# Performance work log

Measured on AMD Instinct MI355X. Metric: run time of the kernel, lower is better.

Reference implementation:

```python
import jax, jax.numpy as jnp
import numpy as np

N_EMB = 768
HEAD_SIZE = 64
B, T = 256, 256


def setup_inputs() -> dict:
    key = jax.random.key(0)
    kx, kq, kk, kv = jax.random.split(key, 4)
    x = jax.random.normal(kx, (B, T, N_EMB), dtype=jnp.float32)
    # nn.Linear(n_emb, head_size, bias=False): store as [in, out], apply x @ W
    s = 1.0 / np.sqrt(N_EMB)
    Wq = jax.random.uniform(kq, (N_EMB, HEAD_SIZE), jnp.float32, -s, s)
    Wk = jax.random.uniform(kk, (N_EMB, HEAD_SIZE), jnp.float32, -s, s)
    Wv = jax.random.uniform(kv, (N_EMB, HEAD_SIZE), jnp.float32, -s, s)
    return {"x": x, "Wq": Wq, "Wk": Wk, "Wv": Wv}


def reference(x, Wq, Wk, Wv):
    # x: [B, T, C]
    q = x @ Wq  # [B, T, H]
    k = x @ Wk  # [B, T, H]
    v = x @ Wv  # [B, T, H]
    scale = k.shape[-1] ** (-0.5)
    wei = jnp.einsum('bth,bsh->bts', q, k) * scale  # [B, T, T]
    t = x.shape[1]
    causal = jnp.tril(jnp.ones((t, t), dtype=bool))  # [T, T]
    wei = jnp.where(causal, wei, -jnp.inf)
    wei = jax.nn.softmax(wei, axis=-1)
    out = jnp.einsum('bts,bsh->bth', wei, v)  # [B, T, H]
    return out
```

## Files before the change

kernel.cpp:

```cpp
#include <hip/hip_runtime.h>
#include <hip/hip_bf16.h>
#include <stdint.h>


typedef __attribute__((ext_vector_type(8))) short short8;
typedef __attribute__((ext_vector_type(4))) short short4v;
typedef __attribute__((ext_vector_type(4))) float f32x4;

#define MFMA16(a, b, c) __builtin_amdgcn_mfma_f32_16x16x32_bf16(a, b, c, 0, 0, 0)

#define BAR() do { \
  asm volatile("s_waitcnt lgkmcnt(0)" ::: "memory"); \
  __builtin_amdgcn_s_barrier(); \
} while (0)

static __device__ __forceinline__ unsigned short f2bf(float f) {
  union { float f; uint32_t u; } v; v.f = f;
  return (unsigned short)((v.u + 0x7FFFu + ((v.u >> 16) & 1u)) >> 16);
}

__global__ void wt_prep(const float* __restrict__ Wq, const float* __restrict__ Wk,
                        const float* __restrict__ Wv, unsigned short* __restrict__ WtT) {
  int idx = blockIdx.x * 256 + threadIdx.x;
  if (idx >= 147456) return;
  int co = idx & 63;
  int c = (idx >> 6) & 31;
  int itm = idx >> 11;
  int it = itm / 3;
  int m = itm - it * 3;
  const float* W = (m == 0) ? Wq : (m == 1 ? Wk : Wv);
  float v = W[(it * 32 + c) * 64 + co];
  if (m == 0) v *= 0.125f;
  WtT[it * 7680 + (m * 64 + co) * 40 + c] = f2bf(v);
}

#define XS0 0
#define XS1 20480
#define WS0 40960
#define WS1 56320
#define KOFF 71680
#define VOFF 104448

__global__ __launch_bounds__(1024, 1) void fused_head(
    const float* __restrict__ x, const unsigned short* __restrict__ WtT,
    float* __restrict__ out) {
  __shared__ char smem[137216];
  const int tid = threadIdx.x;
  const int w = tid >> 6;
  const int lane = tid & 63;
  const int l15 = lane & 15, g = lane >> 4;
  const int b = blockIdx.x;
  const float* xB = x + (size_t)b * 256 * 768;

  char* xs0 = smem + XS0;
  char* xs1 = smem + XS1;
  char* ws0 = smem + WS0;
  char* ws1 = smem + WS1;

  f32x4 acc[12];
  #pragma unroll
  for (int ct = 0; ct < 12; ++ct) acc[ct] = f32x4{0.f, 0.f, 0.f, 0.f};

  const int sxr = tid >> 3;
  const int sxc = tid & 7;
  const bool stv = (tid < 480);

  float4 xA[2], xPB[2];
  short8 wA[2], wPB[2];

  auto loadX = [&](float4* xr, int kk) {
    #pragma unroll
    for (int p = 0; p < 2; ++p)
      xr[p] = *reinterpret_cast<const float4*>(
          xB + (size_t)(p * 128 + sxr) * 768 + kk + sxc * 4);
  };
  auto loadW = [&](short8* wr, int it) {
    if (stv) {
      const short8* s = reinterpret_cast<const short8*>(WtT + (size_t)it * 7680 + tid * 16);
      wr[0] = s[0]; wr[1] = s[1];
    }
  };
  auto storeX = [&](char* xsb, const float4* xr) {
    #pragma unroll
    for (int p = 0; p < 2; ++p) {
      short4v v;
      v[0] = (short)f2bf(xr[p].x); v[1] = (short)f2bf(xr[p].y);
      v[2] = (short)f2bf(xr[p].z); v[3] = (short)f2bf(xr[p].w);
      *reinterpret_cast<short4v*>(xsb + (p * 128 + sxr) * 80 + sxc * 8) = v;
    }
  };
  auto storeW = [&](char* wsb, const short8* wr) {
    if (stv) {
      *reinterpret_cast<short8*>(wsb + tid * 32) = wr[0];
      *reinterpret_cast<short8*>(wsb + tid * 32 + 16) = wr[1];
    }
  };
  auto compute = [&](const char* xsb, const char* wsb) {
    short8 a0 = *reinterpret_cast<const short8*>(xsb + (w * 16 + l15) * 80 + g * 16);
    #pragma unroll
    for (int ct = 0; ct < 12; ++ct) {
      short8 bb = *reinterpret_cast<const short8*>(wsb + (ct * 16 + l15) * 80 + g * 16);
      acc[ct] = MFMA16(a0, bb, acc[ct]);
    }
  };

  loadX(xA, 0); loadW(wA, 0);
  storeX(xs0, xA); storeW(ws0, wA);
  loadX(xPB, 32); loadW(wPB, 1);
  BAR();

  for (int j = 0; j < 12; ++j) {
    if (2 * j + 2 < 24) { loadX(xA, (2 * j + 2) * 32); loadW(wA, 2 * j + 2); }
    compute(xs0, ws0);
    storeX(xs1, xPB); storeW(ws1, wPB);
    BAR();
    if (2 * j + 3 < 24) { loadX(xPB, (2 * j + 3) * 32); loadW(wPB, 2 * j + 3); }
    compute(xs1, ws1);
    if (2 * j + 2 < 24) { storeX(xs0, xA); storeW(ws0, wA); }
    BAR();
  }

  char* Kl = smem + KOFF;
  char* Vl = smem + VOFF;
  char* Ql = smem;
  #pragma unroll
  for (int ct = 0; ct < 4; ++ct) {
    #pragma unroll
    for (int r = 0; r < 4; ++r) {
      int key = w * 16 + g * 4 + r;
      int h = ct * 16 + l15;
      *reinterpret_cast<unsigned short*>(
          Kl + key * 128 + ((h * 2) ^ ((key & 7) << 4))) = f2bf(acc[4 + ct][r]);
      *reinterpret_cast<unsigned short*>(
          Ql + key * 256 + ((h * 2) ^ ((key & 15) << 4))) = f2bf(acc[ct][r]);
    }
    int h = ct * 16 + l15;
    int t0 = w * 16 + g * 4;
    short4v pv;
    pv[0] = (short)f2bf(acc[8 + ct][0]); pv[1] = (short)f2bf(acc[8 + ct][1]);
    pv[2] = (short)f2bf(acc[8 + ct][2]); pv[3] = (short)f2bf(acc[8 + ct][3]);
    *reinterpret_cast<short4v*>(Vl + h * 512 + ((t0 * 2) ^ ((h & 7) << 4))) = pv;
  }
  BAR();

  short8 qf[2][2];
  if (w < 8) {
    #pragma unroll
    for (int rt = 0; rt < 2; ++rt) {
      const int qrow0 = (rt == 0) ? w * 16 : (15 - w) * 16;
      #pragma unroll
      for (int c = 0; c < 2; ++c) {
        int row = qrow0 + l15;
        qf[rt][c] = *reinterpret_cast<const short8*>(
            Ql + row * 256 + ((c * 64 + g * 16) ^ ((row & 15) << 4)));
      }
    }
  }
  BAR();

  if (w < 8) {
    char* Pw = smem + w * 8192;

    #pragma unroll
    for (int rt = 0; rt < 2; ++rt) {
      const int tile_idx = (rt == 0) ? w : 15 - w;
      const int trow0 = tile_idx * 16;
      const int ntile = tile_idx + 1;
      const int pswz = (l15 & 7) << 4;

      f32x4 s[16];
      #pragma unroll
      for (int t = 0; t < 16; ++t) {
        if (t < ntile) {
          int key = t * 16 + l15;
          int kswz = (key & 7) << 4;
          short8 k0 = *reinterpret_cast<const short8*>(Kl + key * 128 + ((g * 16) ^ kswz));
          short8 k1 = *reinterpret_cast<const short8*>(Kl + key * 128 + ((64 + g * 16) ^ kswz));
          f32x4 a = f32x4{0.f, 0.f, 0.f, 0.f};
          a = MFMA16(k0, qf[rt][0], a);
          a = MFMA16(k1, qf[rt][1], a);
          s[t] = a;
        }
      }

      float sum = 0.f;
      #pragma unroll
      for (int t = 0; t < 16; ++t) {
        if (t < ntile) {
          const bool diag = (t == ntile - 1);
          short4v pk;
          #pragma unroll
          for (int r = 0; r < 4; ++r) {
            float p = __expf(s[t][r]);
            if (diag && (g * 4 + r > l15)) p = 0.f;
            sum += p;
            pk[r] = (short)f2bf(p);
          }
          *reinterpret_cast<short4v*>(Pw + l15 * 512 + ((t * 32 + g * 8) ^ pswz)) = pk;
        }
      }
      if (ntile & 1) {
        *reinterpret_cast<short4v*>(Pw + l15 * 512 + ((ntile * 32 + g * 8) ^ pswz)) =
            short4v{0, 0, 0, 0};
      }
      sum += __shfl_xor(sum, 16);
      sum += __shfl_xor(sum, 32);
      const float inv = 1.0f / sum;

      const int nkc = (ntile + 1) >> 1;
      f32x4 o[4];
      #pragma unroll
      for (int i = 0; i < 4; ++i) o[i] = f32x4{0.f, 0.f, 0.f, 0.f};
      #pragma unroll
      for (int kc = 0; kc < 8; ++kc) {
        if (kc < nkc) {
          short8 pa = *reinterpret_cast<const short8*>(
              Pw + l15 * 512 + ((kc * 64 + g * 16) ^ pswz));
          #pragma unroll
          for (int ht = 0; ht < 4; ++ht) {
            int h = ht * 16 + l15;
            short8 bv = *reinterpret_cast<const short8*>(
                Vl + h * 512 + ((kc * 64 + g * 16) ^ ((h & 7) << 4)));
            o[ht] = MFMA16(bv, pa, o[ht]);
          }
        }
      }

      float* dst = out + ((size_t)b * 256 + trow0 + l15) * 64 + g * 4;
      #pragma unroll
      for (int ht = 0; ht < 4; ++ht) {
        float4 ov;
        ov.x = o[ht][0] * inv; ov.y = o[ht][1] * inv;
        ov.z = o[ht][2] * inv; ov.w = o[ht][3] * inv;
        *reinterpret_cast<float4*>(dst + ht * 16) = ov;
      }
    }
  }
}

extern "C" void kernel_launch(void* const* d_in, const int* in_sizes, int n_in,
                              void* d_out, int out_size, void* d_ws, size_t ws_size,
                              hipStream_t stream) {
  const float* x  = (const float*)d_in[0];
  const float* Wq = (const float*)d_in[1];
  const float* Wk = (const float*)d_in[2];
  const float* Wv = (const float*)d_in[3];
  unsigned short* WtT = (unsigned short*)d_ws;
  float* out = (float*)d_out;

  hipLaunchKernelGGL(wt_prep, dim3(576), dim3(256), 0, stream, Wq, Wk, Wv, WtT);
  hipLaunchKernelGGL(fused_head, dim3(256), dim3(1024), 0, stream, x, WtT, out);
}
```

Measured before the change: 51.14 us.

## Split fused head into separate projection and attention kernels via global bf16 buffers

Replaces the single fused 1024-thread-per-batch kernel with a projection kernel and an attention kernel. The projection kernel handles 128 rows per block across 512 blocks, writing Q, K and transposed V as bf16 to workspace. The attention kernel, with 512 threads per batch, reloads them into LDS. This is meant to raise occupancy and parallelism in the projection phase, where 256 single-occupancy blocks underfill the GPU and half the waves sat idle during attention. In exchange it adds a global round trip of Q/K/V and an extra kernel launch.

```diff
diff --git a/kernel.cpp b/kernel.cpp
--- a/kernel.cpp
+++ b/kernel.cpp
@@ -17,6 +17,15 @@
 static __device__ __forceinline__ unsigned short f2bf(float f) {
   union { float f; uint32_t u; } v; v.f = f;
   return (unsigned short)((v.u + 0x7FFFu + ((v.u >> 16) & 1u)) >> 16);
+}
+
+static __device__ __forceinline__ short8 conv8(float4 lo, float4 hi) {
+  short8 a;
+  a[0] = (short)f2bf(lo.x); a[1] = (short)f2bf(lo.y);
+  a[2] = (short)f2bf(lo.z); a[3] = (short)f2bf(lo.w);
+  a[4] = (short)f2bf(hi.x); a[5] = (short)f2bf(hi.y);
+  a[6] = (short)f2bf(hi.z); a[7] = (short)f2bf(hi.w);
+  return a;
 }
 
 __global__ void wt_prep(const float* __restrict__ Wq, const float* __restrict__ Wk,
@@ -34,45 +43,37 @@
   WtT[it * 7680 + (m * 64 + co) * 40 + c] = f2bf(v);
 }
 
-#define XS0 0
-#define XS1 20480
-#define WS0 40960
-#define WS1 56320
-#define KOFF 71680
-#define VOFF 104448
-
-__global__ __launch_bounds__(1024, 1) void fused_head(
+__global__ __launch_bounds__(512, 4) void proj_kernel(
     const float* __restrict__ x, const unsigned short* __restrict__ WtT,
-    float* __restrict__ out) {
-  __shared__ char smem[137216];
+    unsigned short* __restrict__ Q, unsigned short* __restrict__ Kb,
+    unsigned short* __restrict__ Vt) {
+  __shared__ char smem[51200];
+  char* xs_[2] = { smem, smem + 10240 };
+  char* ws_[2] = { smem + 20480, smem + 35840 };
+
   const int tid = threadIdx.x;
-  const int w = tid >> 6;
-  const int lane = tid & 63;
+  const int w = tid >> 6, lane = tid & 63;
   const int l15 = lane & 15, g = lane >> 4;
-  const int b = blockIdx.x;
-  const float* xB = x + (size_t)b * 256 * 768;
-
-  char* xs0 = smem + XS0;
-  char* xs1 = smem + XS1;
-  char* ws0 = smem + WS0;
-  char* ws1 = smem + WS1;
+  const int bid = blockIdx.x;
+  const int b = bid >> 1;
+  const int row0 = (bid & 1) * 128;
+  const float* xB = x + ((size_t)b * 256 + row0) * 768;
 
   f32x4 acc[12];
   #pragma unroll
   for (int ct = 0; ct < 12; ++ct) acc[ct] = f32x4{0.f, 0.f, 0.f, 0.f};
 
-  const int sxr = tid >> 3;
-  const int sxc = tid & 7;
+  const int sxr = tid >> 2;
+  const int sxc = tid & 3;
   const bool stv = (tid < 480);
 
   float4 xA[2], xPB[2];
   short8 wA[2], wPB[2];
 
   auto loadX = [&](float4* xr, int kk) {
-    #pragma unroll
-    for (int p = 0; p < 2; ++p)
-      xr[p] = *reinterpret_cast<const float4*>(
-          xB + (size_t)(p * 128 + sxr) * 768 + kk + sxc * 4);
+    const float* src = xB + (size_t)sxr * 768 + kk + sxc * 8;
+    xr[0] = *reinterpret_cast<const float4*>(src);
+    xr[1] = *reinterpret_cast<const float4*>(src + 4);
   };
   auto loadW = [&](short8* wr, int it) {
     if (stv) {
@@ -81,13 +82,7 @@
     }
   };
   auto storeX = [&](char* xsb, const float4* xr) {
-    #pragma unroll
-    for (int p = 0; p < 2; ++p) {
-      short4v v;
-      v[0] = (short)f2bf(xr[p].x); v[1] = (short)f2bf(xr[p].y);
-      v[2] = (short)f2bf(xr[p].z); v[3] = (short)f2bf(xr[p].w);
-      *reinterpret_cast<short4v*>(xsb + (p * 128 + sxr) * 80 + sxc * 8) = v;
-    }
+    *reinterpret_cast<short8*>(xsb + sxr * 80 + sxc * 16) = conv8(xr[0], xr[1]);
   };
   auto storeW = [&](char* wsb, const short8* wr) {
     if (stv) {
@@ -105,135 +100,157 @@
   };
 
   loadX(xA, 0); loadW(wA, 0);
-  storeX(xs0, xA); storeW(ws0, wA);
+  storeX(xs_[0], xA); storeW(ws_[0], wA);
   loadX(xPB, 32); loadW(wPB, 1);
   BAR();
 
   for (int j = 0; j < 12; ++j) {
     if (2 * j + 2 < 24) { loadX(xA, (2 * j + 2) * 32); loadW(wA, 2 * j + 2); }
-    compute(xs0, ws0);
-    storeX(xs1, xPB); storeW(ws1, wPB);
+    compute(xs_[0], ws_[0]);
+    storeX(xs_[1], xPB); storeW(ws_[1], wPB);
     BAR();
     if (2 * j + 3 < 24) { loadX(xPB, (2 * j + 3) * 32); loadW(wPB, 2 * j + 3); }
-    compute(xs1, ws1);
-    if (2 * j + 2 < 24) { storeX(xs0, xA); storeW(ws0, wA); }
+    compute(xs_[1], ws_[1]);
+    if (2 * j + 2 < 24) { storeX(xs_[0], xA); storeW(ws_[0], wA); }
     BAR();
   }
+
+  {
+    const int trow_l = row0 + w * 16 + g * 4;
+    #pragma unroll
+    for (int ct = 0; ct < 4; ++ct) {
+      #pragma unroll
+      for (int r = 0; r < 4; ++r) {
+        size_t base = ((size_t)b * 256 + trow_l + r) * 64 + l15;
+        Q[base + ct * 16] = f2bf(acc[ct][r]);
+        Kb[base + ct * 16] = f2bf(acc[4 + ct][r]);
+      }
+      int h = ct * 16 + l15;
+      short4v pv;
+      pv[0] = (short)f2bf(acc[8 + ct][0]); pv[1] = (short)f2bf(acc[8 + ct][1]);
+      pv[2] = (short)f2bf(acc[8 + ct][2]); pv[3] = (short)f2bf(acc[8 + ct][3]);
+      *reinterpret_cast<short4v*>(&Vt[((size_t)b * 64 + h) * 256 + trow_l]) = pv;
+    }
+  }
+}
+
+#define KOFF 65536
+#define VOFF 98304
+__global__ __launch_bounds__(512, 2) void attn_kernel(
+    const unsigned short* __restrict__ Q, const unsigned short* __restrict__ Kb,
+    const unsigned short* __restrict__ Vt, float* __restrict__ out) {
+  __shared__ char smem[131072];
+  const int tid = threadIdx.x;
+  const int w = tid >> 6, lane = tid & 63;
+  const int l15 = lane & 15, g = lane >> 4;
+  const int b = blockIdx.x;
 
   char* Kl = smem + KOFF;
   char* Vl = smem + VOFF;
-  char* Ql = smem;
+
+  {
+    int key = tid >> 1, h0 = (tid & 1) * 32;
+    const short8* src = reinterpret_cast<const short8*>(
+        Kb + ((size_t)b * 256 + key) * 64 + h0);
+    int swz = (key & 7) << 4;
+    #pragma unroll
+    for (int j = 0; j < 4; ++j)
+      *reinterpret_cast<short8*>(Kl + key * 128 + (((h0 + j * 8) * 2) ^ swz)) = src[j];
+  }
+  {
+    int h = tid >> 3, t0 = (tid & 7) * 32;
+    const short8* src = reinterpret_cast<const short8*>(
+        Vt + ((size_t)b * 64 + h) * 256 + t0);
+    int swz = (h & 7) << 4;
+    #pragma unroll
+    for (int j = 0; j < 4; ++j)
+      *reinterpret_cast<short8*>(Vl + h * 512 + ((t0 * 2 + j * 16) ^ swz)) = src[j];
+  }
+  short8 qf[2][2];
   #pragma unroll
-  for (int ct = 0; ct < 4; ++ct) {
-    #pragma unroll
-    for (int r = 0; r < 4; ++r) {
-      int key = w * 16 + g * 4 + r;
-      int h = ct * 16 + l15;
-      *reinterpret_cast<unsigned short*>(
-          Kl + key * 128 + ((h * 2) ^ ((key & 7) << 4))) = f2bf(acc[4 + ct][r]);
-      *reinterpret_cast<unsigned short*>(
-          Ql + key * 256 + ((h * 2) ^ ((key & 15) << 4))) = f2bf(acc[ct][r]);
-    }
-    int h = ct * 16 + l15;
-    int t0 = w * 16 + g * 4;
-    short4v pv;
-    pv[0] = (short)f2bf(acc[8 + ct][0]); pv[1] = (short)f2bf(acc[8 + ct][1]);
-    pv[2] = (short)f2bf(acc[8 + ct][2]); pv[3] = (short)f2bf(acc[8 + ct][3]);
-    *reinterpret_cast<short4v*>(Vl + h * 512 + ((t0 * 2) ^ ((h & 7) << 4))) = pv;
+  for (int rt = 0; rt < 2; ++rt) {
+    const int qrow0 = (rt == 0) ? w * 16 : (15 - w) * 16;
+    const short8* qsrc = reinterpret_cast<const short8*>(
+        Q + ((size_t)b * 256 + qrow0 + l15) * 64 + g * 8);
+    qf[rt][0] = qsrc[0];
+    qf[rt][1] = qsrc[4];
   }
   BAR();
 
-  short8 qf[2][2];
-  if (w < 8) {
-    #pragma unroll
-    for (int rt = 0; rt < 2; ++rt) {
-      const int qrow0 = (rt == 0) ? w * 16 : (15 - w) * 16;
-      #pragma unroll
-      for (int c = 0; c < 2; ++c) {
-        int row = qrow0 + l15;
-        qf[rt][c] = *reinterpret_cast<const short8*>(
-            Ql + row * 256 + ((c * 64 + g * 16) ^ ((row & 15) << 4)));
-      }
-    }
-  }
-  BAR();
-
-  if (w < 8) {
-    char* Pw = smem + w * 8192;
-
-    #pragma unroll
-    for (int rt = 0; rt < 2; ++rt) {
-      const int tile_idx = (rt == 0) ? w : 15 - w;
-      const int trow0 = tile_idx * 16;
-      const int ntile = tile_idx + 1;
-      const int pswz = (l15 & 7) << 4;
-
-      f32x4 s[16];
-      #pragma unroll
-      for (int t = 0; t < 16; ++t) {
-        if (t < ntile) {
-          int key = t * 16 + l15;
-          int kswz = (key & 7) << 4;
-          short8 k0 = *reinterpret_cast<const short8*>(Kl + key * 128 + ((g * 16) ^ kswz));
-          short8 k1 = *reinterpret_cast<const short8*>(Kl + key * 128 + ((64 + g * 16) ^ kswz));
-          f32x4 a = f32x4{0.f, 0.f, 0.f, 0.f};
-          a = MFMA16(k0, qf[rt][0], a);
-          a = MFMA16(k1, qf[rt][1], a);
-          s[t] = a;
+  char* Pw = smem + w * 8192;
+
+  #pragma unroll
+  for (int rt = 0; rt < 2; ++rt) {
+    const int tile_idx = (rt == 0) ? w : 15 - w;
+    const int trow0 = tile_idx * 16;
+    const int ntile = tile_idx + 1;
+    const int pswz = (l15 & 7) << 4;
+
+    f32x4 s[16];
+    #pragma unroll
+    for (int t = 0; t < 16; ++t) {
+      if (t < ntile) {
+        int key = t * 16 + l15;
+        int kswz = (key & 7) << 4;
+        short8 k0 = *reinterpret_cast<const short8*>(Kl + key * 128 + ((g * 16) ^ kswz));
+        short8 k1 = *reinterpret_cast<const short8*>(Kl + key * 128 + ((64 + g * 16) ^ kswz));
+        f32x4 a = f32x4{0.f, 0.f, 0.f, 0.f};
+        a = MFMA16(k0, qf[rt][0], a);
+        a = MFMA16(k1, qf[rt][1], a);
+        s[t] = a;
+      }
+    }
+
+    float sum = 0.f;
+    #pragma unroll
+    for (int t = 0; t < 16; ++t) {
+      if (t < ntile) {
+        const bool diag = (t == ntile - 1);
+        short4v pk;
+        #pragma unroll
+        for (int r = 0; r < 4; ++r) {
+          float p = __expf(s[t][r]);
+          if (diag && (g * 4 + r > l15)) p = 0.f;
+          sum += p;
+          pk[r] = (short)f2bf(p);
         }
-      }
-
-      float sum = 0.f;
-      #pragma unroll
-      for (int t = 0; t < 16; ++t) {
-        if (t < ntile) {
-          const bool diag = (t == ntile - 1);
-          short4v pk;
-          #pragma unroll
-          for (int r = 0; r < 4; ++r) {
-            float p = __expf(s[t][r]);
-            if (diag && (g * 4 + r > l15)) p = 0.f;
-            sum += p;
-            pk[r] = (short)f2bf(p);
-          }
-          *reinterpret_cast<short4v*>(Pw + l15 * 512 + ((t * 32 + g * 8) ^ pswz)) = pk;
+        *reinterpret_cast<short4v*>(Pw + l15 * 512 + ((t * 32 + g * 8) ^ pswz)) = pk;
+      }
+    }
+    if (ntile & 1) {
+      *reinterpret_cast<short4v*>(Pw + l15 * 512 + ((ntile * 32 + g * 8) ^ pswz)) =
+          short4v{0, 0, 0, 0};
+    }
+    sum += __shfl_xor(sum, 16);
+    sum += __shfl_xor(sum, 32);
+    const float inv = 1.0f / sum;
+
+    const int nkc = (ntile + 1) >> 1;
+    f32x4 o[4];
+    #pragma unroll
+    for (int i = 0; i < 4; ++i) o[i] = f32x4{0.f, 0.f, 0.f, 0.f};
+    #pragma unroll
+    for (int kc = 0; kc < 8; ++kc) {
+      if (kc < nkc) {
+        short8 pa = *reinterpret_cast<const short8*>(
+            Pw + l15 * 512 + ((kc * 64 + g * 16) ^ pswz));
+        #pragma unroll
+        for (int ht = 0; ht < 4; ++ht) {
+          int h = ht * 16 + l15;
+          short8 bv = *reinterpret_cast<const short8*>(
+              Vl + h * 512 + ((kc * 64 + g * 16) ^ ((h & 7) << 4)));
+          o[ht] = MFMA16(bv, pa, o[ht]);
         }
       }
-      if (ntile & 1) {
-        *reinterpret_cast<short4v*>(Pw + l15 * 512 + ((ntile * 32 + g * 8) ^ pswz)) =
-            short4v{0, 0, 0, 0};
-      }
-      sum += __shfl_xor(sum, 16);
-      sum += __shfl_xor(sum, 32);
-      const float inv = 1.0f / sum;
-
-      const int nkc = (ntile + 1) >> 1;
-      f32x4 o[4];
-      #pragma unroll
-      for (int i = 0; i < 4; ++i) o[i] = f32x4{0.f, 0.f, 0.f, 0.f};
-      #pragma unroll
-      for (int kc = 0; kc < 8; ++kc) {
-        if (kc < nkc) {
-          short8 pa = *reinterpret_cast<const short8*>(
-              Pw + l15 * 512 + ((kc * 64 + g * 16) ^ pswz));
-          #pragma unroll
-          for (int ht = 0; ht < 4; ++ht) {
-            int h = ht * 16 + l15;
-            short8 bv = *reinterpret_cast<const short8*>(
-                Vl + h * 512 + ((kc * 64 + g * 16) ^ ((h & 7) << 4)));
-            o[ht] = MFMA16(bv, pa, o[ht]);
-          }
-        }
-      }
-
-      float* dst = out + ((size_t)b * 256 + trow0 + l15) * 64 + g * 4;
-      #pragma unroll
-      for (int ht = 0; ht < 4; ++ht) {
-        float4 ov;
-        ov.x = o[ht][0] * inv; ov.y = o[ht][1] * inv;
-        ov.z = o[ht][2] * inv; ov.w = o[ht][3] * inv;
-        *reinterpret_cast<float4*>(dst + ht * 16) = ov;
-      }
+    }
+
+    float* dst = out + ((size_t)b * 256 + trow0 + l15) * 64 + g * 4;
+    #pragma unroll
+    for (int ht = 0; ht < 4; ++ht) {
+      float4 ov;
+      ov.x = o[ht][0] * inv; ov.y = o[ht][1] * inv;
+      ov.z = o[ht][2] * inv; ov.w = o[ht][3] * inv;
+      *reinterpret_cast<float4*>(dst + ht * 16) = ov;
     }
   }
 }
@@ -245,9 +262,14 @@
   const float* Wq = (const float*)d_in[1];
   const float* Wk = (const float*)d_in[2];
   const float* Wv = (const float*)d_in[3];
-  unsigned short* WtT = (unsigned short*)d_ws;
+  char* ws = (char*)d_ws;
+  unsigned short* WtT = (unsigned short*)ws;
+  unsigned short* Q   = (unsigned short*)(ws + 393216);
+  unsigned short* Kb  = (unsigned short*)(ws + 393216 + 8388608);
+  unsigned short* Vt  = (unsigned short*)(ws + 393216 + 2 * 8388608);
   float* out = (float*)d_out;
 
   hipLaunchKernelGGL(wt_prep, dim3(576), dim3(256), 0, stream, Wq, Wk, Wv, WtT);
-  hipLaunchKernelGGL(fused_head, dim3(256), dim3(1024), 0, stream, x, WtT, out);
-}
+  hipLaunchKernelGGL(proj_kernel, dim3(512), dim3(512), 0, stream, x, WtT, Q, Kb, Vt);
+  hipLaunchKernelGGL(attn_kernel, dim3(256), dim3(512), 0, stream, Q, Kb, Vt, out);
+}
```

Measured after the change: 58.94 us. +15.2%, slower.
